# Kernel tuning notes

Hardware: AMD Instinct MI355X
Metric: run time of the kernel (lower is better)

## Reference

```python
import jax, jax.numpy as jnp
import numpy as np

N = 100000   # nodes
E = 1600000  # edges
IN = 128     # in_node_channels
H = 128      # hidden_channels
EPS = 1e-5   # BatchNorm eps


def _gcn_conv(x, W, b, src, dst, n):
    # x' = W x, then symmetric-normalized aggregation with self-loops (PyG GCNConv)
    xw = x @ W                                             # [N, H]
    loop = jnp.arange(n, dtype=src.dtype)
    src_f = jnp.concatenate([src, loop])                   # [E+N]
    dst_f = jnp.concatenate([dst, loop])
    deg = jax.ops.segment_sum(jnp.ones(src_f.shape, xw.dtype), dst_f, num_segments=n)
    dis = jax.lax.rsqrt(jnp.maximum(deg, 1.0))             # deg >= 1 due to self-loops
    norm = dis[src_f] * dis[dst_f]                         # [E+N]
    msg = xw[src_f] * norm[:, None]                        # gather + scale
    out = jax.ops.segment_sum(msg, dst_f, num_segments=n)  # scatter-add
    return out + b


def _bn(x, gamma, beta):
    # training-mode BatchNorm1d over the node dimension
    m = jnp.mean(x, axis=0)
    v = jnp.mean(jnp.square(x - m), axis=0)
    return gamma * (x - m) * jax.lax.rsqrt(v + EPS) + beta


def setup_inputs() -> dict:
    key = jax.random.key(0)
    ks = jax.random.split(key, 8)
    glorot = lambda k, shape, fan: jax.random.normal(k, shape, jnp.float32) / np.sqrt(fan).astype(np.float32)
    x = jax.random.normal(ks[0], (N, IN), jnp.float32)
    edge_index = jax.random.randint(ks[1], (2, E), 0, N, dtype=jnp.int32)
    return {
        "x": x,
        "edge_index": edge_index,
        "W1": glorot(ks[2], (IN, H), IN), "b1": jnp.zeros((H,), jnp.float32),
        "g1": jnp.ones((H,), jnp.float32), "be1": jnp.zeros((H,), jnp.float32),
        "W2": glorot(ks[3], (H, H), H), "b2": jnp.zeros((H,), jnp.float32),
        "g2": jnp.ones((H,), jnp.float32), "be2": jnp.zeros((H,), jnp.float32),
        "Wm1": glorot(ks[4], (H, 64), H), "bm1": jnp.zeros((64,), jnp.float32),
        "Wm2": glorot(ks[5], (64, 1), 64), "bm2": jnp.zeros((1,), jnp.float32),
    }


def reference(x, edge_index, W1, b1, g1, be1, W2, b2, g2, be2, Wm1, bm1, Wm2, bm2):
    src, dst = edge_index[0], edge_index[1]
    h = jax.nn.relu(_bn(_gcn_conv(x, W1, b1, src, dst, N), g1, be1))
    h = jax.nn.relu(_bn(_gcn_conv(h, W2, b2, src, dst, N), g2, be2))
    # MLP head (dropout is identity in eval / deterministic reference)
    h = jax.nn.relu(h @ Wm1 + bm1)
    out = h @ Wm2 + bm2                                     # [N, 1]
    return jnp.squeeze(out, axis=-1)                        # [N]
```

## Files before the change

kernel.cpp:

```cpp
#include <hip/hip_runtime.h>
#include <hip/hip_fp16.h>

#define HC 128
#define EPS_BN 1e-5f
#define NSTRIPE 8
#define AGG_BLOCKS 3072
#define BSHIFT 9
#define BNODES (1 << BSHIFT)
#define CHUNK 8192
#define SRC_BITS 18

typedef _Float16 f16;
typedef f16  f16x8 __attribute__((ext_vector_type(8)));
typedef float f32x4 __attribute__((ext_vector_type(4)));

__global__ __launch_bounds__(1024) void bucket_count(const int* __restrict__ dst,
                                                     int* __restrict__ bcnt, int E) {
    __shared__ int c[256];
    const int tid = threadIdx.x;
    const int e0 = blockIdx.x * CHUNK;
    if (tid < 256) c[tid] = 0;
    __syncthreads();
    for (int i = tid; i < CHUNK; i += 1024) {
        int e = e0 + i;
        if (e < E) atomicAdd(&c[dst[e] >> BSHIFT], 1);
    }
    __syncthreads();
    if (tid < 256 && c[tid] > 0) atomicAdd(&bcnt[tid], c[tid]);
}

__global__ __launch_bounds__(256) void bscan(const int* __restrict__ bcnt,
                                             int* __restrict__ bbase, int* __restrict__ gcur,
                                             int* __restrict__ rowptr, int nb, int n, int E) {
    __shared__ int s[256];
    const int tid = threadIdx.x;
    s[tid] = (tid < nb) ? bcnt[tid] : 0;
    __syncthreads();
    for (int off = 1; off < 256; off <<= 1) {
        int t = (tid >= off) ? s[tid - off] : 0;
        __syncthreads();
        s[tid] += t;
        __syncthreads();
    }
    int excl = tid ? s[tid - 1] : 0;
    if (tid < nb) { bbase[tid] = excl; gcur[tid] = excl; }
    if (tid == 0) { bbase[nb] = E; rowptr[n] = E; }
}

__global__ __launch_bounds__(1024) void edge_bin(const int* __restrict__ src,
                                                 const int* __restrict__ dst,
                                                 int* __restrict__ gcur,
                                                 unsigned int* __restrict__ packed, int E) {
    __shared__ int cnt[256];
    __shared__ int cur[256];
    const int tid = threadIdx.x;
    const int e0 = blockIdx.x * CHUNK;
    if (tid < 256) cnt[tid] = 0;
    __syncthreads();
    for (int i = tid; i < CHUNK; i += 1024) {
        int e = e0 + i;
        if (e < E) atomicAdd(&cnt[dst[e] >> BSHIFT], 1);
    }
    __syncthreads();
    if (tid < 256) cur[tid] = (cnt[tid] > 0) ? atomicAdd(&gcur[tid], cnt[tid]) : 0;
    __syncthreads();
    for (int i = tid; i < CHUNK; i += 1024) {
        int e = e0 + i;
        if (e < E) {
            int s = src[e], d = dst[e];
            int pos = atomicAdd(&cur[d >> BSHIFT], 1);
            packed[pos] = ((unsigned)(d & (BNODES - 1)) << SRC_BITS) | (unsigned)s;
        }
    }
}

__global__ __launch_bounds__(1024) void edge_sort(const unsigned int* __restrict__ packed,
                                                  const int* __restrict__ bbase,
                                                  int* __restrict__ rowptr,
                                                  float* __restrict__ dis,
                                                  int* __restrict__ srcs, int n) {
    __shared__ int cnt[BNODES];
    __shared__ int cur[BNODES];
    __shared__ int scn[BNODES];
    const int b = blockIdx.x;
    const int node0 = b << BSHIFT;
    const int tid = threadIdx.x;
    const int base = bbase[b];
    const int end  = bbase[b + 1];

    if (tid < BNODES) cnt[tid] = 0;
    __syncthreads();
    for (int e = base + tid; e < end; e += 1024)
        atomicAdd(&cnt[packed[e] >> SRC_BITS], 1);
    __syncthreads();
    if (tid < BNODES) scn[tid] = cnt[tid];
    __syncthreads();
    for (int off = 1; off < BNODES; off <<= 1) {
        int t = 0;
        if (tid < BNODES && tid >= off) t = scn[tid - off];
        __syncthreads();
        if (tid < BNODES) scn[tid] += t;
        __syncthreads();
    }
    if (tid < BNODES) {
        int excl = scn[tid] - cnt[tid];
        int node = node0 + tid;
        if (node < n) {
            rowptr[node] = base + excl;
            dis[node] = rsqrtf((float)cnt[tid] + 1.f);
        }
        cur[tid] = excl;
    }
    __syncthreads();
    for (int e = base + tid; e < end; e += 1024) {
        unsigned p = packed[e];
        int pos = atomicAdd(&cur[p >> SRC_BITS], 1);
        srcs[base + pos] = (int)(p & ((1u << SRC_BITS) - 1));
    }
}

__global__ void wprep_all(const float* __restrict__ W1, const float* __restrict__ W2,
                          const float* __restrict__ Wm1,
                          f16* __restrict__ Wt1, f16* __restrict__ Wt2,
                          f16* __restrict__ Wm1t, f16* __restrict__ padrow) {
    int idx = blockIdx.x * 256 + threadIdx.x;
    if (idx < 16384) {
        int k = idx >> 7, c = idx & 127;
        Wt1[(size_t)c * HC + k] = (f16)W1[idx];
    } else if (idx < 32768) {
        int i = idx - 16384;
        int k = i >> 7, c = i & 127;
        Wt2[(size_t)c * HC + k] = (f16)W2[i];
    } else if (idx < 40960) {
        int i = idx - 32768;
        int c = i >> 7, k = i & 127;
        Wm1t[(size_t)c * HC + k] = (f16)Wm1[(size_t)k * 64 + c];
    } else if (idx < 41088) {
        padrow[idx - 40960] = (f16)0.f;
    }
}

template<int SRC_F16, int TRANS>
__global__ __launch_bounds__(256) void gemm_mfma(const void* __restrict__ Xv,
                                                 const f16* __restrict__ Wt,
                                                 const float* __restrict__ stats,
                                                 const float* __restrict__ gamma,
                                                 const float* __restrict__ beta,
                                                 const float* __restrict__ dis,
                                                 f16* __restrict__ Y, int n) {
    __shared__ f16 Ah[64][136];
    __shared__ f16 Bh[128][136];
    __shared__ float sc[HC], sh[HC];
    const int tid  = threadIdx.x;
    const int row0 = blockIdx.x * 64;

    if constexpr (TRANS) {
        if (tid < 128) {
            float s = 0.f, q = 0.f;
#pragma unroll
            for (int t = 0; t < NSTRIPE; ++t) {
                s += stats[t * 256 + tid];
                q += stats[t * 256 + 128 + tid];
            }
            float m = s / (float)n;
            float v = q / (float)n - m * m;
            float scv = gamma[tid] * rsqrtf(fmaxf(v, 0.f) + EPS_BN);
            sc[tid] = scv;
            sh[tid] = beta[tid] - m * scv;
        }
    }

#pragma unroll
    for (int i = 0; i < 8; ++i) {
        int idx = i * 256 + tid;
        int r = idx >> 4, g = idx & 15;
        *(f16x8*)&Bh[r][g * 8] = *(const f16x8*)(Wt + (size_t)r * HC + g * 8);
    }
    __syncthreads();

#pragma unroll
    for (int i = 0; i < 4; ++i) {
        int idx = i * 256 + tid;
        int r = idx >> 4, g = idx & 15;
        int grow = row0 + r;
        f16x8 h = {};
        if (grow < n) {
            if constexpr (SRC_F16) {
                f16x8 v = *(const f16x8*)((const f16*)Xv + (size_t)grow * HC + g * 8);
                if constexpr (TRANS) {
#pragma unroll
                    for (int j = 0; j < 8; ++j) {
                        float f = (float)v[j];
                        f = fmaxf(fmaf(f, sc[g * 8 + j], sh[g * 8 + j]), 0.f);
                        h[j] = (f16)f;
                    }
                } else h = v;
            } else {
                const float* X = (const float*)Xv;
                float4 a = *(const float4*)(X + (size_t)grow * HC + g * 8);
                float4 c = *(const float4*)(X + (size_t)grow * HC + g * 8 + 4);
                h[0] = (f16)a.x; h[1] = (f16)a.y; h[2] = (f16)a.z; h[3] = (f16)a.w;
                h[4] = (f16)c.x; h[5] = (f16)c.y; h[6] = (f16)c.z; h[7] = (f16)c.w;
            }
        }
        *(f16x8*)&Ah[r][g * 8] = h;
    }
    __syncthreads();

    const int wv   = tid >> 6;
    const int lane = tid & 63;
    const int m    = lane & 15;
    const int kq   = (lane >> 4) * 8;

    f32x4 acc[8] = {};
#pragma unroll
    for (int kc = 0; kc < HC; kc += 32) {
        f16x8 a = *(const f16x8*)&Ah[wv * 16 + m][kc + kq];
#pragma unroll
        for (int t = 0; t < 8; ++t) {
            f16x8 b = *(const f16x8*)&Bh[t * 16 + m][kc + kq];
            acc[t] = __builtin_amdgcn_mfma_f32_16x16x32_f16(a, b, acc[t], 0, 0, 0);
        }
    }

    const int rbase = row0 + wv * 16 + (lane >> 4) * 4;
#pragma unroll
    for (int r = 0; r < 4; ++r) {
        int grow = rbase + r;
        if (grow < n) {
            float dv = dis[grow];
#pragma unroll
            for (int t = 0; t < 8; ++t)
                Y[(size_t)grow * HC + t * 16 + m] = (f16)(acc[t][r] * dv);
        }
    }
}

__global__ __launch_bounds__(256) void gcn_agg_f16(const f16* __restrict__ xws,
                                                   const int* __restrict__ srcs,
                                                   const int* __restrict__ rowptr,
                                                   const float* __restrict__ dis,
                                                   const float* __restrict__ bias,
                                                   f16* __restrict__ out,
                                                   float* __restrict__ stats,
                                                   int n, int nwaves) {
    __shared__ float lds_s[4][128], lds_q[4][128];
    const int wv   = threadIdx.x >> 6;
    const int lane = threadIdx.x & 63;
    const int g    = lane >> 4;
    const int cg   = lane & 15;

    float b8[8];
#pragma unroll
    for (int j = 0; j < 8; ++j) b8[j] = bias[cg * 8 + j];

    float s8[8] = {}, q8[8] = {};

    for (int node = blockIdx.x * 4 + wv; node < n; node += nwaves) {
        const int e0 = rowptr[node];
        const int e1 = rowptr[node + 1];
        float acc[8] = {};
        for (int e = e0; e < e1; e += 8) {
            int i0 = e + g, i1 = e + g + 4;
            int s0 = (i0 < e1) ? srcs[i0] : n;
            int s1 = (i1 < e1) ? srcs[i1] : n;
            f16x8 v0 = *(const f16x8*)(xws + (size_t)s0 * HC + cg * 8);
            f16x8 v1 = *(const f16x8*)(xws + (size_t)s1 * HC + cg * 8);
#pragma unroll
            for (int j = 0; j < 8; ++j) {
                acc[j] += (float)v0[j];
                acc[j] += (float)v1[j];
            }
        }
#pragma unroll
        for (int j = 0; j < 8; ++j) acc[j] += __shfl_xor(acc[j], 16);
#pragma unroll
        for (int j = 0; j < 8; ++j) acc[j] += __shfl_xor(acc[j], 32);

        if (g == 0) {
            float dv = dis[node];
            f16x8 self = *(const f16x8*)(xws + (size_t)node * HC + cg * 8);
            f16x8 o;
#pragma unroll
            for (int j = 0; j < 8; ++j) {
                float r = fmaf(acc[j] + (float)self[j], dv, b8[j]);
                o[j] = (f16)r;
                s8[j] += r;
                q8[j] += r * r;
            }
            *(f16x8*)(out + (size_t)node * HC + cg * 8) = o;
        }
    }

    if (g == 0) {
#pragma unroll
        for (int j = 0; j < 8; ++j) {
            lds_s[wv][cg * 8 + j] = s8[j];
            lds_q[wv][cg * 8 + j] = q8[j];
        }
    }
    __syncthreads();
    float* stripe = stats + (size_t)(blockIdx.x & (NSTRIPE - 1)) * 256;
    if (threadIdx.x < 128) {
        float s = lds_s[0][threadIdx.x] + lds_s[1][threadIdx.x] +
                  lds_s[2][threadIdx.x] + lds_s[3][threadIdx.x];
        float q = lds_q[0][threadIdx.x] + lds_q[1][threadIdx.x] +
                  lds_q[2][threadIdx.x] + lds_q[3][threadIdx.x];
        atomicAdd(&stripe[threadIdx.x], s);
        atomicAdd(&stripe[128 + threadIdx.x], q);
    }
}

__global__ __launch_bounds__(256) void mlp_mfma(const f16* __restrict__ h,
                                                const float* __restrict__ stats,
                                                const float* __restrict__ gamma,
                                                const float* __restrict__ beta,
                                                const f16* __restrict__ Wm1t,
                                                const float* __restrict__ bm1,
                                                const float* __restrict__ Wm2,
                                                const float* __restrict__ bm2,
                                                float* __restrict__ out, int n) {
    __shared__ f16 Hs[64][136];
    __shared__ f16 Ws[64][136];
    __shared__ float sc[HC], sh[HC], bmv[64], w2v[64];
    const int tid  = threadIdx.x;
    const int row0 = blockIdx.x * 64;

    if (tid < 128) {
        float s = 0.f, q = 0.f;
#pragma unroll
        for (int t = 0; t < NSTRIPE; ++t) {
            s += stats[t * 256 + tid];
            q += stats[t * 256 + 128 + tid];
        }
        float m = s / (float)n;
        float v = q / (float)n - m * m;
        float scv = gamma[tid] * rsqrtf(fmaxf(v, 0.f) + EPS_BN);
        sc[tid] = scv;
        sh[tid] = beta[tid] - m * scv;
    }
    if (tid < 64) { bmv[tid] = bm1[tid]; w2v[tid] = Wm2[tid]; }

#pragma unroll
    for (int i = 0; i < 4; ++i) {
        int idx = i * 256 + tid;
        int r = idx >> 4, g = idx & 15;
        *(f16x8*)&Ws[r][g * 8] = *(const f16x8*)(Wm1t + (size_t)r * HC + g * 8);
    }
    __syncthreads();

#pragma unroll
    for (int i = 0; i < 4; ++i) {
        int idx = i * 256 + tid;
        int r = idx >> 4, g = idx & 15;
        int grow = row0 + r;
        f16x8 hv = {};
        if (grow < n) {
            f16x8 v = *(const f16x8*)(h + (size_t)grow * HC + g * 8);
#pragma unroll
            for (int j = 0; j < 8; ++j) {
                float f = (float)v[j];
                f = fmaxf(fmaf(f, sc[g * 8 + j], sh[g * 8 + j]), 0.f);
                hv[j] = (f16)f;
            }
        }
        *(f16x8*)&Hs[r][g * 8] = hv;
    }
    __syncthreads();

    const int wv   = tid >> 6;
    const int lane = tid & 63;
    const int m    = lane & 15;
    const int kq   = (lane >> 4) * 8;

    f32x4 acc[4] = {};
#pragma unroll
    for (int kc = 0; kc < HC; kc += 32) {
        f16x8 a = *(const f16x8*)&Hs[wv * 16 + m][kc + kq];
#pragma unroll
        for (int t = 0; t < 4; ++t) {
            f16x8 b = *(const f16x8*)&Ws[t * 16 + m][kc + kq];
            acc[t] = __builtin_amdgcn_mfma_f32_16x16x32_f16(a, b, acc[t], 0, 0, 0);
        }
    }

    float part[4];
#pragma unroll
    for (int reg = 0; reg < 4; ++reg) {
        float s = 0.f;
#pragma unroll
        for (int t = 0; t < 4; ++t) {
            int col = t * 16 + m;
            s += fmaxf(acc[t][reg] + bmv[col], 0.f) * w2v[col];
        }
        part[reg] = s;
    }
#pragma unroll
    for (int off = 1; off < 16; off <<= 1) {
#pragma unroll
        for (int reg = 0; reg < 4; ++reg)
            part[reg] += __shfl_xor(part[reg], off);
    }
    if (m == 0) {
        int rbase = row0 + wv * 16 + (lane >> 4) * 4;
        float bb = bm2[0];
#pragma unroll
        for (int reg = 0; reg < 4; ++reg) {
            int row = rbase + reg;
            if (row < n) out[row] = part[reg] + bb;
        }
    }
}

extern "C" void kernel_launch(void* const* d_in, const int* in_sizes, int n_in,
                              void* d_out, int out_size, void* d_ws, size_t ws_size,
                              hipStream_t stream) {
    const float* x   = (const float*)d_in[0];
    const int*   ei  = (const int*)  d_in[1];
    const float* W1  = (const float*)d_in[2];
    const float* b1  = (const float*)d_in[3];
    const float* g1  = (const float*)d_in[4];
    const float* be1 = (const float*)d_in[5];
    const float* W2  = (const float*)d_in[6];
    const float* b2  = (const float*)d_in[7];
    const float* g2  = (const float*)d_in[8];
    const float* be2 = (const float*)d_in[9];
    const float* Wm1 = (const float*)d_in[10];
    const float* bm1 = (const float*)d_in[11];
    const float* Wm2 = (const float*)d_in[12];
    const float* bm2 = (const float*)d_in[13];
    float* out = (float*)d_out;

    const int n = in_sizes[0] / HC;
    const int E = in_sizes[1] / 2;
    const int* srcp = ei;
    const int* dstp = ei + E;
    const int nb = (n + BNODES - 1) >> BSHIFT;

    char* ws = (char*)d_ws;
    size_t off = 0;
    auto alloc = [&](size_t bytes) { void* p = ws + off; off = (off + bytes + 511) & ~511ULL; return p; };
    float*  dis    = (float*) alloc((size_t)n * 4);
    int*    rowptr = (int*)   alloc((size_t)(n + 1) * 4);
    int*    zreg   = (int*)   alloc((256 + 2 * NSTRIPE * 256) * 4);
    int*    bcnt   = zreg;
    float*  stats1 = (float*)(zreg + 256);
    float*  stats2 = stats1 + NSTRIPE * 256;
    int*    bbase  = (int*)   alloc(1024 + 4);
    int*    gcur   = (int*)   alloc(1024);
    unsigned int* packed = (unsigned int*)alloc((size_t)E * 4);
    int*    srcs   = (int*)   alloc((size_t)E * 4);
    f16*    xws    = (f16*)   alloc((size_t)(n + 1) * HC * 2);
    f16*    bufBh  = (f16*)   alloc((size_t)n * HC * 2);
    f16*    Wt1    = (f16*)   alloc((size_t)HC * HC * 2);
    f16*    Wt2    = (f16*)   alloc((size_t)HC * HC * 2);
    f16*    Wm1t   = (f16*)   alloc((size_t)64 * HC * 2);

    const int gemmBlocks = (n + 63) / 64;
    const int binBlocks  = (E + CHUNK - 1) / CHUNK;
    const int aggWaves   = AGG_BLOCKS * 4;

    hipMemsetAsync(zreg, 0, (256 + 2 * NSTRIPE * 256) * 4, stream);

    bucket_count<<<binBlocks, 1024, 0, stream>>>(dstp, bcnt, E);
    bscan<<<1, 256, 0, stream>>>(bcnt, bbase, gcur, rowptr, nb, n, E);
    edge_bin<<<binBlocks, 1024, 0, stream>>>(srcp, dstp, gcur, packed, E);
    edge_sort<<<nb, 1024, 0, stream>>>(packed, bbase, rowptr, dis, srcs, n);

    wprep_all<<<(41088 + 255) / 256, 256, 0, stream>>>(W1, W2, Wm1, Wt1, Wt2, Wm1t,
                                                       xws + (size_t)n * HC);

    gemm_mfma<0, 0><<<gemmBlocks, 256, 0, stream>>>(x, Wt1, nullptr, nullptr, nullptr,
                                                    dis, xws, n);
    gcn_agg_f16<<<AGG_BLOCKS, 256, 0, stream>>>(xws, srcs, rowptr, dis, b1,
                                                bufBh, stats1, n, aggWaves);

    gemm_mfma<1, 1><<<gemmBlocks, 256, 0, stream>>>(bufBh, Wt2, stats1, g1, be1,
                                                    dis, xws, n);
    gcn_agg_f16<<<AGG_BLOCKS, 256, 0, stream>>>(xws, srcs, rowptr, dis, b2,
                                                bufBh, stats2, n, aggWaves);

    mlp_mfma<<<gemmBlocks, 256, 0, stream>>>(bufBh, stats2, g2, be2, Wm1t, bm1, Wm2, bm2,
                                             out, n);
}
```

Baseline: 329.6 us.

## Slice feature matrix into 16-channel column panels for cache-local aggregation

The GEMM output is stored as eight column slices of 16 channels each, laid out node-major within each slice, instead of a dense row-major N x 128 matrix. The aggregation kernel assigns each block to one slice, so gathers for a slice touch a table of about 3.2 MB that can stay resident in L2/LLC rather than the full 25.6 MB table. Each edge is fetched as two 16-byte halves by 8 lanes per node, and the BN stats reduction is adjusted to the per-slice channel mapping. In exchange, the source indices are read eight times (once per slice), and the GEMM stores become strided across slices.

After: 409.1 us. 1.24x slower.

```diff
diff --git a/kernel.cpp b/kernel.cpp
--- a/kernel.cpp
+++ b/kernel.cpp
@@ -122,7 +122,8 @@
 __global__ void wprep_all(const float* __restrict__ W1, const float* __restrict__ W2,
                           const float* __restrict__ Wm1,
                           f16* __restrict__ Wt1, f16* __restrict__ Wt2,
-                          f16* __restrict__ Wm1t, f16* __restrict__ padrow) {
+                          f16* __restrict__ Wm1t, f16* __restrict__ xws,
+                          int n, int sstride16) {
     int idx = blockIdx.x * 256 + threadIdx.x;
     if (idx < 16384) {
         int k = idx >> 7, c = idx & 127;
@@ -136,7 +137,9 @@
         int c = i >> 7, k = i & 127;
         Wm1t[(size_t)c * HC + k] = (f16)Wm1[(size_t)k * 64 + c];
     } else if (idx < 41088) {
-        padrow[idx - 40960] = (f16)0.f;
+        int i = idx - 40960;
+        int slice = i >> 4, j = i & 15;
+        xws[(size_t)slice * sstride16 + (size_t)n * 16 + j] = (f16)0.f;
     }
 }
 
@@ -147,7 +150,7 @@
                                                  const float* __restrict__ gamma,
                                                  const float* __restrict__ beta,
                                                  const float* __restrict__ dis,
-                                                 f16* __restrict__ Y, int n) {
+                                                 f16* __restrict__ Y, int n, int sstride16) {
     __shared__ f16 Ah[64][136];
     __shared__ f16 Bh[128][136];
     __shared__ float sc[HC], sh[HC];
@@ -231,55 +234,59 @@
             float dv = dis[grow];
 #pragma unroll
             for (int t = 0; t < 8; ++t)
-                Y[(size_t)grow * HC + t * 16 + m] = (f16)(acc[t][r] * dv);
-        }
-    }
-}
-
-__global__ __launch_bounds__(256) void gcn_agg_f16(const f16* __restrict__ xws,
-                                                   const int* __restrict__ srcs,
-                                                   const int* __restrict__ rowptr,
-                                                   const float* __restrict__ dis,
-                                                   const float* __restrict__ bias,
-                                                   f16* __restrict__ out,
-                                                   float* __restrict__ stats,
-                                                   int n, int nwaves) {
-    __shared__ float lds_s[4][128], lds_q[4][128];
-    const int wv   = threadIdx.x >> 6;
-    const int lane = threadIdx.x & 63;
-    const int g    = lane >> 4;
-    const int cg   = lane & 15;
+                Y[(size_t)t * sstride16 + (size_t)grow * 16 + m] = (f16)(acc[t][r] * dv);
+        }
+    }
+}
+
+__global__ __launch_bounds__(256) void gcn_agg_sl(const f16* __restrict__ xws,
+                                                  const int* __restrict__ srcs,
+                                                  const int* __restrict__ rowptr,
+                                                  const float* __restrict__ dis,
+                                                  const float* __restrict__ bias,
+                                                  f16* __restrict__ out,
+                                                  float* __restrict__ stats,
+                                                  int n, int sstride16) {
+    __shared__ float lds_s[4][4][2][8], lds_q[4][4][2][8];
+    const int tid   = threadIdx.x;
+    const int wv    = tid >> 6;
+    const int lane  = tid & 63;
+    const int npos  = lane >> 4;
+    const int ei    = (lane >> 1) & 7;
+    const int h     = lane & 1;
+    const int slice = blockIdx.x & 7;
+    const int blkSl = blockIdx.x >> 3;
+    const int nodeStride = (AGG_BLOCKS >> 3) * 16;
+
+    const f16* xsl = xws + (size_t)slice * sstride16;
 
     float b8[8];
 #pragma unroll
-    for (int j = 0; j < 8; ++j) b8[j] = bias[cg * 8 + j];
+    for (int j = 0; j < 8; ++j) b8[j] = bias[slice * 16 + h * 8 + j];
 
     float s8[8] = {}, q8[8] = {};
 
-    for (int node = blockIdx.x * 4 + wv; node < n; node += nwaves) {
-        const int e0 = rowptr[node];
-        const int e1 = rowptr[node + 1];
+    for (int nb = (blkSl * 4 + wv) * 4 + npos; nb < n; nb += nodeStride) {
+        const int e0 = rowptr[nb];
+        const int e1 = rowptr[nb + 1];
         float acc[8] = {};
         for (int e = e0; e < e1; e += 8) {
-            int i0 = e + g, i1 = e + g + 4;
-            int s0 = (i0 < e1) ? srcs[i0] : n;
-            int s1 = (i1 < e1) ? srcs[i1] : n;
-            f16x8 v0 = *(const f16x8*)(xws + (size_t)s0 * HC + cg * 8);
-            f16x8 v1 = *(const f16x8*)(xws + (size_t)s1 * HC + cg * 8);
-#pragma unroll
-            for (int j = 0; j < 8; ++j) {
-                acc[j] += (float)v0[j];
-                acc[j] += (float)v1[j];
-            }
-        }
-#pragma unroll
-        for (int j = 0; j < 8; ++j) acc[j] += __shfl_xor(acc[j], 16);
-#pragma unroll
-        for (int j = 0; j < 8; ++j) acc[j] += __shfl_xor(acc[j], 32);
-
-        if (g == 0) {
-            float dv = dis[node];
-            f16x8 self = *(const f16x8*)(xws + (size_t)node * HC + cg * 8);
+            int idx = e + ei;
+            int s = (idx < e1) ? srcs[idx] : n;
+            f16x8 v = *(const f16x8*)(xsl + (size_t)s * 16 + h * 8);
+#pragma unroll
+            for (int j = 0; j < 8; ++j) acc[j] += (float)v[j];
+        }
+#pragma unroll
+        for (int j = 0; j < 8; ++j) acc[j] += __shfl_xor(acc[j], 2);
+#pragma unroll
+        for (int j = 0; j < 8; ++j) acc[j] += __shfl_xor(acc[j], 4);
+#pragma unroll
+        for (int j = 0; j < 8; ++j) acc[j] += __shfl_xor(acc[j], 8);
+
+        if (ei == 0) {
+            float dv = dis[nb];
+            f16x8 self = *(const f16x8*)(xsl + (size_t)nb * 16 + h * 8);
             f16x8 o;
 #pragma unroll
             for (int j = 0; j < 8; ++j) {
@@ -288,26 +295,32 @@
                 s8[j] += r;
                 q8[j] += r * r;
             }
-            *(f16x8*)(out + (size_t)node * HC + cg * 8) = o;
-        }
-    }
-
-    if (g == 0) {
+            *(f16x8*)(out + (size_t)nb * HC + slice * 16 + h * 8) = o;
+        }
+    }
+
+    if (ei == 0) {
 #pragma unroll
         for (int j = 0; j < 8; ++j) {
-            lds_s[wv][cg * 8 + j] = s8[j];
-            lds_q[wv][cg * 8 + j] = q8[j];
-        }
-    }
-    __syncthreads();
-    float* stripe = stats + (size_t)(blockIdx.x & (NSTRIPE - 1)) * 256;
-    if (threadIdx.x < 128) {
-        float s = lds_s[0][threadIdx.x] + lds_s[1][threadIdx.x] +
-                  lds_s[2][threadIdx.x] + lds_s[3][threadIdx.x];
-        float q = lds_q[0][threadIdx.x] + lds_q[1][threadIdx.x] +
-                  lds_q[2][threadIdx.x] + lds_q[3][threadIdx.x];
-        atomicAdd(&stripe[threadIdx.x], s);
-        atomicAdd(&stripe[128 + threadIdx.x], q);
+            lds_s[wv][npos][h][j] = s8[j];
+            lds_q[wv][npos][h][j] = q8[j];
+        }
+    }
+    __syncthreads();
+    if (tid < 16) {
+        int hh = tid >> 3, j = tid & 7;
+        float s = 0.f, q = 0.f;
+#pragma unroll
+        for (int w = 0; w < 4; ++w)
+#pragma unroll
+            for (int p = 0; p < 4; ++p) {
+                s += lds_s[w][p][hh][j];
+                q += lds_q[w][p][hh][j];
+            }
+        int ch = slice * 16 + hh * 8 + j;
+        float* stripe = stats + (size_t)((blockIdx.x >> 3) & (NSTRIPE - 1)) * 256;
+        atomicAdd(&stripe[ch], s);
+        atomicAdd(&stripe[128 + ch], q);
     }
 }
 
@@ -436,6 +449,7 @@
     const int* srcp = ei;
     const int* dstp = ei + E;
     const int nb = (n + BNODES - 1) >> BSHIFT;
+    const int sstride16 = (n + 1) * 16;
 
     char* ws = (char*)d_ws;
     size_t off = 0;
@@ -450,7 +464,7 @@
     int*    gcur   = (int*)   alloc(1024);
     unsigned int* packed = (unsigned int*)alloc((size_t)E * 4);
     int*    srcs   = (int*)   alloc((size_t)E * 4);
-    f16*    xws    = (f16*)   alloc((size_t)(n + 1) * HC * 2);
+    f16*    xws    = (f16*)   alloc((size_t)8 * sstride16 * 2);
     f16*    bufBh  = (f16*)   alloc((size_t)n * HC * 2);
     f16*    Wt1    = (f16*)   alloc((size_t)HC * HC * 2);
     f16*    Wt2    = (f16*)   alloc((size_t)HC * HC * 2);
@@ -458,7 +472,6 @@
 
     const int gemmBlocks = (n + 63) / 64;
     const int binBlocks  = (E + CHUNK - 1) / CHUNK;
-    const int aggWaves   = AGG_BLOCKS * 4;
 
     hipMemsetAsync(zreg, 0, (256 + 2 * NSTRIPE * 256) * 4, stream);
 
@@ -468,17 +481,17 @@
     edge_sort<<<nb, 1024, 0, stream>>>(packed, bbase, rowptr, dis, srcs, n);
 
     wprep_all<<<(41088 + 255) / 256, 256, 0, stream>>>(W1, W2, Wm1, Wt1, Wt2, Wm1t,
-                                                       xws + (size_t)n * HC);
+                                                       xws, n, sstride16);
 
     gemm_mfma<0, 0><<<gemmBlocks, 256, 0, stream>>>(x, Wt1, nullptr, nullptr, nullptr,
-                                                    dis, xws, n);
-    gcn_agg_f16<<<AGG_BLOCKS, 256, 0, stream>>>(xws, srcs, rowptr, dis, b1,
-                                                bufBh, stats1, n, aggWaves);
+                                                    dis, xws, n, sstride16);
+    gcn_agg_sl<<<AGG_BLOCKS, 256, 0, stream>>>(xws, srcs, rowptr, dis, b1,
+                                               bufBh, stats1, n, sstride16);
 
     gemm_mfma<1, 1><<<gemmBlocks, 256, 0, stream>>>(bufBh, Wt2, stats1, g1, be1,
-                                                    dis, xws, n);
-    gcn_agg_f16<<<AGG_BLOCKS, 256, 0, stream>>>(xws, srcs, rowptr, dis, b2,
-                                                bufBh, stats2, n, aggWaves);
+                                                    dis, xws, n, sstride16);
+    gcn_agg_sl<<<AGG_BLOCKS, 256, 0, stream>>>(xws, srcs, rowptr, dis, b2,
+                                               bufBh, stats2, n, sstride16);
 
     mlp_mfma<<<gemmBlocks, 256, 0, stream>>>(bufBh, stats2, g2, be2, Wm1t, bm1, Wm2, bm2,
                                              out, n);
```
